# Performance work log

Measured on AMD Instinct MI355X. Metric: run time of the kernel, lower is better.

Reference implementation:

```python
import jax, jax.numpy as jnp
import numpy as np

N_E = 8192
E_DIM = 512
BETA = 0.25


def setup_inputs() -> dict:
    key = jax.random.key(0)
    k1, k2, k3, k4 = jax.random.split(key, 4)
    x = jax.random.normal(k1, (32, 512, E_DIM), dtype=jnp.float32)
    label = jax.random.randint(k2, (32, 512), 0, 100, dtype=jnp.int64)
    idx = jax.random.randint(k3, (32, 512), 0, 512, dtype=jnp.int64)
    # codebook initialized uniform(-1/n_e, 1/n_e) as in the torch module
    W = jax.random.uniform(k4, (N_E, E_DIM), dtype=jnp.float32,
                           minval=-1.0 / N_E, maxval=1.0 / N_E)
    return {"x": x, "label": label, "idx": idx, "W": W}


def reference(x, label, idx, W):
    # label/idx are unused in the forward math (mirrors the torch module)
    latent = x.reshape(-1, E_DIM)                        # [N, e_dim]
    # squared euclidean distances: ||z||^2 + ||c||^2 - 2 z c^T
    d = (jnp.sum(latent ** 2, axis=1, keepdims=True)
         + jnp.sum(W ** 2, axis=1)[None, :]
         - 2.0 * jnp.matmul(latent, W.T))                # [N, n_e]
    indices = jnp.argmin(d, axis=-1)                     # [N]
    x_q = W[indices].reshape(x.shape)                    # gather + reshape
    commitment_loss = jnp.mean((jax.lax.stop_gradient(x_q) - x) ** 2)
    loss = BETA * commitment_loss
    # straight-through estimator
    x_q = x + jax.lax.stop_gradient(x_q - x)
    indices = indices.reshape(x.shape[:-1])
    return x_q, loss, indices
```

## Files before the change

kernel.cpp:

```cpp
#include <hip/hip_runtime.h>
#include <cstdint>
#include <cstddef>

#define EDIM  512
#define NROWS 16384
#define NE    8192
#define XQSZ  (NROWS * EDIM)
#define NTILE 64
#define K3    1536

#define OFF_PART  0
#define OFF_Z     16384
#define OFF_C2    81920
#define OFF_KEYS  114688
#define OFF_TMIN  245760
#define OFF_CNT   4440064
#define OFF_LIST  4441088
#define OFF_XE    8635392
#define OFF_WE    58967040

typedef __attribute__((ext_vector_type(8)))  short          short8;
typedef __attribute__((ext_vector_type(16))) float          f32x16;
typedef __attribute__((ext_vector_type(4)))  unsigned short u16x4;

__global__ void k_rownorm(const float* __restrict__ in, float* __restrict__ out, int nrows) {
#pragma clang fp contract(off)
    int row = blockIdx.x * blockDim.x + threadIdx.x;
    if (row >= nrows) return;
    const float* p = in + (size_t)row * EDIM;
    float S[4];
#pragma unroll
    for (int b = 0; b < 4; ++b) {
        const float* q = p + b * 128;
        float r[8];
#pragma unroll
        for (int j = 0; j < 8; ++j) { float v = q[j]; r[j] = v * v; }
        for (int i = 8; i < 128; i += 8) {
#pragma unroll
            for (int j = 0; j < 8; ++j) { float v = q[i + j]; r[j] = r[j] + v * v; }
        }
        S[b] = ((r[0] + r[1]) + (r[2] + r[3])) + ((r[4] + r[5]) + (r[6] + r[7]));
    }
    out[row] = (S[0] + S[1]) + (S[2] + S[3]);
}

__device__ __forceinline__ unsigned short f2bf(float f) {
    unsigned u = __float_as_uint(f);
    return (unsigned short)((u + 0x7FFFu + ((u >> 16) & 1u)) >> 16);
}
__device__ __forceinline__ float bf2f(unsigned short h) {
    return __uint_as_float(((unsigned)h) << 16);
}

__global__ __launch_bounds__(256) void k_split3(const float* __restrict__ in,
        unsigned short* __restrict__ outp, int nrows) {
    int e = blockIdx.x * 256 + threadIdx.x;
    int row = e >> 7;
    int d0  = (e & 127) << 2;
    if (row >= nrows) return;
    float4 v = *(const float4*)(in + (size_t)row * EDIM + d0);
    float vv[4] = {v.x, v.y, v.z, v.w};
    u16x4 H, M, L;
#pragma unroll
    for (int i = 0; i < 4; ++i) {
        float f = vv[i];
        unsigned short h = f2bf(f);
        float r1 = f - bf2f(h);
        unsigned short m = f2bf(r1);
        float r2 = r1 - bf2f(m);
        L[i] = f2bf(r2); H[i] = h; M[i] = m;
    }
    unsigned short* o = outp + (size_t)row * K3 + d0;
    *(u16x4*)(o) = H; *(u16x4*)(o + EDIM) = M; *(u16x4*)(o + 2 * EDIM) = L;
}

__device__ __forceinline__ void gld16(const void* g, void* l) {
    __builtin_amdgcn_global_load_lds((const __attribute__((address_space(1))) void*)g,
                                     (__attribute__((address_space(3))) void*)l, 16, 0, 0);
}

#define GBM 128
#define GBN 128
#define GBK 64

__global__ __launch_bounds__(256) void k_argmin_hi(
        const unsigned short* __restrict__ Xe, const unsigned short* __restrict__ We,
        const float* __restrict__ c2, unsigned* __restrict__ tmin) {
    __shared__ __align__(16) unsigned short At[GBM * GBK];
    __shared__ __align__(16) unsigned short Bt[GBN * GBK];
    __shared__ unsigned smin[GBM];
    __shared__ float cs[GBN];

    const int tid = threadIdx.x;
    const int lane = tid & 63, wid = tid >> 6;
    const int wr = wid >> 1, wc = wid & 1;

    const int bid = blockIdx.x;
    const int swz = (bid & 7) * 1024 + (bid >> 3);
    const int rowtile = swz & 127, codetile = swz >> 7;
    const int row0 = rowtile * GBM, code0 = codetile * GBN;

    if (tid < GBM) smin[tid] = 0xFFFFFFFFu;
    if (tid < GBN) cs[tid] = 4.0f + c2[code0 + tid];

    f32x16 acc[2][2];
#pragma unroll
    for (int i = 0; i < 2; ++i)
#pragma unroll
        for (int j = 0; j < 2; ++j)
#pragma unroll
            for (int r = 0; r < 16; ++r) acc[i][j][r] = 0.0f;

    size_t ga[4], gb[4];
#pragma unroll
    for (int i = 0; i < 4; ++i) {
        int chunk = i * 256 + tid;
        int row   = chunk >> 3;
        int kcs   = (chunk & 7) ^ (row & 7);
        ga[i] = (size_t)(row0 + row) * K3 + kcs * 8;
        gb[i] = (size_t)(code0 + row) * K3 + kcs * 8;
    }

    const int cb0 = wr * 64 + (lane & 31);
    const int xa0 = wc * 64 + (lane & 31);
    const int kh  = lane >> 5;
    const int sb  = cb0 & 7, sa = xa0 & 7;

    for (int kt = 0; kt < EDIM / GBK; ++kt) {
        const size_t ko = (size_t)kt * GBK;
#pragma unroll
        for (int i = 0; i < 4; ++i) {
            gld16(Xe + ga[i] + ko, (char*)At + i * 4096 + wid * 1024);
            gld16(We + gb[i] + ko, (char*)Bt + i * 4096 + wid * 1024);
        }
        __syncthreads();
#pragma unroll
        for (int ks = 0; ks < 4; ++ks) {
            const int ch = ks * 2 + kh;
            short8 c0 = *(const short8*)((const char*)Bt + cb0 * 128        + ((ch ^ sb) * 16));
            short8 c1 = *(const short8*)((const char*)Bt + (cb0 + 32) * 128 + ((ch ^ sb) * 16));
            short8 x0 = *(const short8*)((const char*)At + xa0 * 128        + ((ch ^ sa) * 16));
            short8 x1 = *(const short8*)((const char*)At + (xa0 + 32) * 128 + ((ch ^ sa) * 16));
            acc[0][0] = __builtin_amdgcn_mfma_f32_32x32x16_bf16(c0, x0, acc[0][0], 0, 0, 0);
            acc[0][1] = __builtin_amdgcn_mfma_f32_32x32x16_bf16(c0, x1, acc[0][1], 0, 0, 0);
            acc[1][0] = __builtin_amdgcn_mfma_f32_32x32x16_bf16(c1, x0, acc[1][0], 0, 0, 0);
            acc[1][1] = __builtin_amdgcn_mfma_f32_32x32x16_bf16(c1, x1, acc[1][1], 0, 0, 0);
        }
        __syncthreads();
    }

    const int kh4 = kh * 4;
#pragma unroll
    for (int nj = 0; nj < 2; ++nj) {
        float dmin = 3.4e38f;
#pragma unroll
        for (int mi = 0; mi < 2; ++mi) {
#pragma unroll
            for (int q = 0; q < 4; ++q) {
                const float4 cq = *(const float4*)&cs[wr * 64 + mi * 32 + q * 8 + kh4];
                dmin = fminf(dmin, fmaf(-2.0f, acc[mi][nj][q * 4 + 0], cq.x));
                dmin = fminf(dmin, fmaf(-2.0f, acc[mi][nj][q * 4 + 1], cq.y));
                dmin = fminf(dmin, fmaf(-2.0f, acc[mi][nj][q * 4 + 2], cq.z));
                dmin = fminf(dmin, fmaf(-2.0f, acc[mi][nj][q * 4 + 3], cq.w));
            }
        }
        const int xr = wc * 64 + nj * 32 + (lane & 31);
        atomicMin(&smin[xr], __float_as_uint(dmin));
    }
    __syncthreads();
    if (tid < GBM) tmin[codetile * NROWS + row0 + tid] = smin[tid];
}

__global__ __launch_bounds__(256) void k_select(
        const unsigned* __restrict__ tmin, const float* __restrict__ Z,
        int* __restrict__ cnt, int* __restrict__ list) {
    const int row = blockIdx.x * 256 + threadIdx.x;
    unsigned mn = 0xFFFFFFFFu;
    for (int t = 0; t < NTILE; ++t) {
        unsigned v = tmin[t * NROWS + row];
        if (v < mn) mn = v;
    }
    const float margin = 4.35e-5f * sqrtf(Z[row]) + 1.7e-4f;
    const float thr = __uint_as_float(mn) + margin;
    for (int t = 0; t < NTILE; ++t) {
        if (__uint_as_float(tmin[t * NROWS + row]) <= thr) {
            int p = atomicAdd(&cnt[t], 1);
            list[t * NROWS + p] = row;
        }
    }
}

__global__ __launch_bounds__(256) void k_rescore_mfma(
        const unsigned short* __restrict__ Xe, const unsigned short* __restrict__ We,
        const float* __restrict__ Z, const float* __restrict__ c2,
        const int* __restrict__ cnt, const int* __restrict__ list,
        unsigned long long* __restrict__ keys) {
    __shared__ __align__(16) unsigned short At[GBM * GBK];
    __shared__ __align__(16) unsigned short Bt[GBN * GBK];
    __shared__ int rl_s[GBM];
    __shared__ float Zs[GBM];
    __shared__ float cs2[GBN];

    const int tile = blockIdx.x;
    const int n = cnt[tile];
    if (n == 0) return;
    const int* rows = list + tile * NROWS;
    const int tid = threadIdx.x;
    const int lane = tid & 63, wid = tid >> 6;
    const int wr = wid >> 1, wc = wid & 1;
    const int code0 = tile * 128;

    if (tid < GBN) cs2[tid] = c2[code0 + tid];

    const int cb0 = wr * 64 + (lane & 31);
    const int xa0 = wc * 64 + (lane & 31);
    const int kh  = lane >> 5;
    const int kh4 = kh * 4;
    const int sb  = cb0 & 7, sa = xa0 & 7;

    for (int chk = (int)blockIdx.y; chk * GBM < n; chk += 16) {
        __syncthreads();
        if (tid < GBM) {
            int ri = chk * GBM + tid;
            int r = rows[ri < n ? ri : 0];
            rl_s[tid] = r;
            Zs[tid] = Z[r];
        }
        __syncthreads();

        size_t aoff[4], boff[4];
#pragma unroll
        for (int i = 0; i < 4; ++i) {
            int chunk = i * 256 + tid;
            int row   = chunk >> 3;
            int kcs   = (chunk & 7) ^ (row & 7);
            aoff[i] = (size_t)rl_s[row] * K3 + kcs * 8;
            boff[i] = (size_t)(code0 + row) * K3 + kcs * 8;
        }

        f32x16 acc[2][2];
#pragma unroll
        for (int i = 0; i < 2; ++i)
#pragma unroll
            for (int j = 0; j < 2; ++j)
#pragma unroll
                for (int r = 0; r < 16; ++r) acc[i][j][r] = 0.0f;

#pragma unroll
        for (int bt = 0; bt < 6; ++bt) {
            const int ao = (bt == 1 || bt == 2) ? EDIM : (bt == 4 ? 2 * EDIM : 0);
            const int bo = (bt == 0 || bt == 2) ? EDIM : (bt == 3 ? 2 * EDIM : 0);
            for (int kc = 0; kc < 8; ++kc) {
                const int ko = ao + kc * GBK;
                const int kob = bo + kc * GBK;
#pragma unroll
                for (int i = 0; i < 4; ++i) {
                    gld16(Xe + aoff[i] + ko,  (char*)At + i * 4096 + wid * 1024);
                    gld16(We + boff[i] + kob, (char*)Bt + i * 4096 + wid * 1024);
                }
                __syncthreads();
#pragma unroll
                for (int ks = 0; ks < 4; ++ks) {
                    const int ch = ks * 2 + kh;
                    short8 c0 = *(const short8*)((const char*)Bt + cb0 * 128        + ((ch ^ sb) * 16));
                    short8 c1 = *(const short8*)((const char*)Bt + (cb0 + 32) * 128 + ((ch ^ sb) * 16));
                    short8 x0 = *(const short8*)((const char*)At + xa0 * 128        + ((ch ^ sa) * 16));
                    short8 x1 = *(const short8*)((const char*)At + (xa0 + 32) * 128 + ((ch ^ sa) * 16));
                    acc[0][0] = __builtin_amdgcn_mfma_f32_32x32x16_bf16(c0, x0, acc[0][0], 0, 0, 0);
                    acc[0][1] = __builtin_amdgcn_mfma_f32_32x32x16_bf16(c0, x1, acc[0][1], 0, 0, 0);
                    acc[1][0] = __builtin_amdgcn_mfma_f32_32x32x16_bf16(c1, x0, acc[1][0], 0, 0, 0);
                    acc[1][1] = __builtin_amdgcn_mfma_f32_32x32x16_bf16(c1, x1, acc[1][1], 0, 0, 0);
                }
                __syncthreads();
            }
        }

#pragma unroll
        for (int nj = 0; nj < 2; ++nj) {
            const int xr = wc * 64 + nj * 32 + (lane & 31);
            const float Zr = Zs[xr];
            float dm = 3.4e38f; int jm = 0;
#pragma unroll
            for (int mi = 0; mi < 2; ++mi) {
#pragma unroll
                for (int q = 0; q < 4; ++q) {
                    const float4 cq = *(const float4*)&cs2[wr * 64 + mi * 32 + q * 8 + kh4];
                    const int jb = code0 + wr * 64 + mi * 32 + q * 8 + kh4;
                    { const float d = (Zr + cq.x) - 2.0f * acc[mi][nj][q * 4 + 0];
                      if (d < dm) { dm = d; jm = jb + 0; } }
                    { const float d = (Zr + cq.y) - 2.0f * acc[mi][nj][q * 4 + 1];
                      if (d < dm) { dm = d; jm = jb + 1; } }
                    { const float d = (Zr + cq.z) - 2.0f * acc[mi][nj][q * 4 + 2];
                      if (d < dm) { dm = d; jm = jb + 2; } }
                    { const float d = (Zr + cq.w) - 2.0f * acc[mi][nj][q * 4 + 3];
                      if (d < dm) { dm = d; jm = jb + 3; } }
                }
            }
            const unsigned long long k =
                (((unsigned long long)__float_as_uint(dm)) << 13) | (unsigned)jm;
            atomicMin(&keys[rl_s[xr]], k);
        }
    }
}

__global__ __launch_bounds__(256) void k_gather(
        const float* __restrict__ x, const float* __restrict__ W,
        const unsigned long long* __restrict__ keys,
        float* __restrict__ out, double* __restrict__ part) {
    const int tid = threadIdx.x;
    const int row = blockIdx.x * 8 + (tid >> 5);
    const int c = tid & 31;
    const int idx = (int)(keys[row] & 0x1FFFull);

    const float* wrow = W + (size_t)idx * EDIM;
    const float* xrow = x + (size_t)row * EDIM;
    float* orow = out + (size_t)row * EDIM;

    double lsum = 0.0;
#pragma unroll
    for (int v = 0; v < 4; ++v) {
        const int d = c * 4 + v * 128;
        float4 xv = *(const float4*)(xrow + d);
        float4 wv = *(const float4*)(wrow + d);
        float t0 = wv.x - xv.x, t1 = wv.y - xv.y, t2 = wv.z - xv.z, t3 = wv.w - xv.w;
        float4 ov = { xv.x + t0, xv.y + t1, xv.z + t2, xv.w + t3 };
        *(float4*)(orow + d) = ov;
        lsum += (double)t0 * t0 + (double)t1 * t1 + (double)t2 * t2 + (double)t3 * t3;
    }
    if (c == 0) out[XQSZ + 1 + row] = (float)idx;

#pragma unroll
    for (int off = 32; off > 0; off >>= 1) lsum += __shfl_down(lsum, off, 64);
    __shared__ double pb[4];
    if ((tid & 63) == 0) pb[tid >> 6] = lsum;
    __syncthreads();
    if (tid == 0) part[blockIdx.x] = pb[0] + pb[1] + pb[2] + pb[3];
}

__global__ __launch_bounds__(256) void k_finalize(float* __restrict__ out,
        const double* __restrict__ part) {
    const int tid = threadIdx.x;
    double s = 0.0;
    for (int i = tid; i < 2048; i += 256) s += part[i];
#pragma unroll
    for (int off = 32; off > 0; off >>= 1) s += __shfl_down(s, off, 64);
    __shared__ double pb[4];
    if ((tid & 63) == 0) pb[tid >> 6] = s;
    __syncthreads();
    if (tid == 0) out[XQSZ] = (float)(0.25 * (pb[0] + pb[1] + pb[2] + pb[3]) / (double)XQSZ);
}

extern "C" void kernel_launch(void* const* d_in, const int* in_sizes, int n_in,
                              void* d_out, int out_size, void* d_ws, size_t ws_size,
                              hipStream_t stream) {
    const float* x = (const float*)d_in[0];
    const float* W = (const float*)d_in[3];
    float* out = (float*)d_out;
    char* ws = (char*)d_ws;

    double* part = (double*)(ws + OFF_PART);
    float* Z    = (float*)(ws + OFF_Z);
    float* c2   = (float*)(ws + OFF_C2);
    unsigned long long* keys = (unsigned long long*)(ws + OFF_KEYS);
    unsigned* tmin = (unsigned*)(ws + OFF_TMIN);
    int* cnt  = (int*)(ws + OFF_CNT);
    int* list = (int*)(ws + OFF_LIST);
    unsigned short* Xe = (unsigned short*)(ws + OFF_XE);
    unsigned short* We = (unsigned short*)(ws + OFF_WE);

    hipMemsetAsync(keys, 0xFF, NROWS * sizeof(unsigned long long), stream);
    hipMemsetAsync(cnt, 0, NTILE * sizeof(int), stream);
    k_rownorm<<<NROWS / 256, 256, 0, stream>>>(x, Z, NROWS);
    k_rownorm<<<NE / 256, 256, 0, stream>>>(W, c2, NE);
    k_split3<<<(NROWS * 128) / 256, 256, 0, stream>>>(x, Xe, NROWS);
    k_split3<<<(NE * 128) / 256, 256, 0, stream>>>(W, We, NE);
    k_argmin_hi<<<(NROWS / GBM) * (NE / GBN), 256, 0, stream>>>(Xe, We, c2, tmin);
    k_select<<<NROWS / 256, 256, 0, stream>>>(tmin, Z, cnt, list);
    k_rescore_mfma<<<dim3(NTILE, 16), 256, 0, stream>>>(Xe, We, Z, c2, cnt, list, keys);
    k_gather<<<NROWS / 8, 256, 0, stream>>>(x, W, keys, out, part);
    k_finalize<<<1, 256, 0, stream>>>(out, part);
}
```

Baseline: 535.6 us.

## Fuse prep kernels into one launch and shrink rescore row tile to 32

Merges the two row-norm and two bf16x3 split kernels into a single k_prep launch that dispatches on block index, removing three kernel launches. The rescore kernel now processes candidate rows in chunks of 32 instead of 128, with each wave owning 32 codes and a single MFMA accumulator. Its epilogue reduces packed distance/index keys with a cross-half shuffle before the atomicMin. Smaller chunks cut wasted padded work when per-tile candidate counts are small. The cost is that the codebook tile is reloaded more often per candidate row, and each MFMA has less operand reuse.

```diff
diff --git a/kernel.cpp b/kernel.cpp
--- a/kernel.cpp
+++ b/kernel.cpp
@@ -23,11 +23,8 @@
 typedef __attribute__((ext_vector_type(16))) float          f32x16;
 typedef __attribute__((ext_vector_type(4)))  unsigned short u16x4;
 
-__global__ void k_rownorm(const float* __restrict__ in, float* __restrict__ out, int nrows) {
+__device__ __forceinline__ float rownorm512(const float* __restrict__ p) {
 #pragma clang fp contract(off)
-    int row = blockIdx.x * blockDim.x + threadIdx.x;
-    if (row >= nrows) return;
-    const float* p = in + (size_t)row * EDIM;
     float S[4];
 #pragma unroll
     for (int b = 0; b < 4; ++b) {
@@ -41,7 +38,7 @@
         }
         S[b] = ((r[0] + r[1]) + (r[2] + r[3])) + ((r[4] + r[5]) + (r[6] + r[7]));
     }
-    out[row] = (S[0] + S[1]) + (S[2] + S[3]);
+    return (S[0] + S[1]) + (S[2] + S[3]);
 }
 
 __device__ __forceinline__ unsigned short f2bf(float f) {
@@ -52,12 +49,10 @@
     return __uint_as_float(((unsigned)h) << 16);
 }
 
-__global__ __launch_bounds__(256) void k_split3(const float* __restrict__ in,
-        unsigned short* __restrict__ outp, int nrows) {
-    int e = blockIdx.x * 256 + threadIdx.x;
+__device__ __forceinline__ void split_group(const float* __restrict__ in,
+        unsigned short* __restrict__ outp, int e) {
     int row = e >> 7;
     int d0  = (e & 127) << 2;
-    if (row >= nrows) return;
     float4 v = *(const float4*)(in + (size_t)row * EDIM + d0);
     float vv[4] = {v.x, v.y, v.z, v.w};
     u16x4 H, M, L;
@@ -72,6 +67,24 @@
     }
     unsigned short* o = outp + (size_t)row * K3 + d0;
     *(u16x4*)(o) = H; *(u16x4*)(o + EDIM) = M; *(u16x4*)(o + 2 * EDIM) = L;
+}
+
+__global__ __launch_bounds__(256) void k_prep(
+        const float* __restrict__ x, const float* __restrict__ W,
+        unsigned short* __restrict__ Xe, unsigned short* __restrict__ We,
+        float* __restrict__ Z, float* __restrict__ c2) {
+    const int bid = blockIdx.x, tid = threadIdx.x;
+    if (bid < 8192) {
+        split_group(x, Xe, bid * 256 + tid);
+    } else if (bid < 12288) {
+        split_group(W, We, (bid - 8192) * 256 + tid);
+    } else if (bid < 12352) {
+        const int row = (bid - 12288) * 256 + tid;
+        Z[row] = rownorm512(x + (size_t)row * EDIM);
+    } else {
+        const int row = (bid - 12352) * 256 + tid;
+        c2[row] = rownorm512(W + (size_t)row * EDIM);
+    }
 }
 
 __device__ __forceinline__ void gld16(const void* g, void* l) {
@@ -195,10 +208,11 @@
         const float* __restrict__ Z, const float* __restrict__ c2,
         const int* __restrict__ cnt, const int* __restrict__ list,
         unsigned long long* __restrict__ keys) {
-    __shared__ __align__(16) unsigned short At[GBM * GBK];
+#define RBM 32
+    __shared__ __align__(16) unsigned short At[RBM * GBK];
     __shared__ __align__(16) unsigned short Bt[GBN * GBK];
-    __shared__ int rl_s[GBM];
-    __shared__ float Zs[GBM];
+    __shared__ int rl_s[RBM];
+    __shared__ float Zs[RBM];
     __shared__ float cs2[GBN];
 
     const int tile = blockIdx.x;
@@ -207,100 +221,81 @@
     const int* rows = list + tile * NROWS;
     const int tid = threadIdx.x;
     const int lane = tid & 63, wid = tid >> 6;
-    const int wr = wid >> 1, wc = wid & 1;
     const int code0 = tile * 128;
 
     if (tid < GBN) cs2[tid] = c2[code0 + tid];
 
-    const int cb0 = wr * 64 + (lane & 31);
-    const int xa0 = wc * 64 + (lane & 31);
-    const int kh  = lane >> 5;
-    const int kh4 = kh * 4;
-    const int sb  = cb0 & 7, sa = xa0 & 7;
-
-    for (int chk = (int)blockIdx.y; chk * GBM < n; chk += 16) {
+    const int cb = wid * 32 + (lane & 31);
+    const int xa = lane & 31;
+    const int kh = lane >> 5;
+    const int sb = cb & 7, sa = xa & 7;
+
+    size_t boff[4];
+#pragma unroll
+    for (int i = 0; i < 4; ++i) {
+        int chunk = i * 256 + tid;
+        int brow  = chunk >> 3;
+        int bkcs  = (chunk & 7) ^ (brow & 7);
+        boff[i] = (size_t)(code0 + brow) * K3 + bkcs * 8;
+    }
+    const int arow = tid >> 3;
+    const int akcs = (tid & 7) ^ (arow & 7);
+
+    for (int chk = (int)blockIdx.y; chk * RBM < n; chk += 16) {
         __syncthreads();
-        if (tid < GBM) {
-            int ri = chk * GBM + tid;
+        if (tid < RBM) {
+            int ri = chk * RBM + tid;
             int r = rows[ri < n ? ri : 0];
             rl_s[tid] = r;
             Zs[tid] = Z[r];
         }
         __syncthreads();
 
-        size_t aoff[4], boff[4];
-#pragma unroll
-        for (int i = 0; i < 4; ++i) {
-            int chunk = i * 256 + tid;
-            int row   = chunk >> 3;
-            int kcs   = (chunk & 7) ^ (row & 7);
-            aoff[i] = (size_t)rl_s[row] * K3 + kcs * 8;
-            boff[i] = (size_t)(code0 + row) * K3 + kcs * 8;
-        }
-
-        f32x16 acc[2][2];
-#pragma unroll
-        for (int i = 0; i < 2; ++i)
-#pragma unroll
-            for (int j = 0; j < 2; ++j)
-#pragma unroll
-                for (int r = 0; r < 16; ++r) acc[i][j][r] = 0.0f;
+        const size_t aoff = (size_t)rl_s[arow] * K3 + akcs * 8;
+
+        f32x16 acc;
+#pragma unroll
+        for (int r = 0; r < 16; ++r) acc[r] = 0.0f;
 
 #pragma unroll
         for (int bt = 0; bt < 6; ++bt) {
             const int ao = (bt == 1 || bt == 2) ? EDIM : (bt == 4 ? 2 * EDIM : 0);
             const int bo = (bt == 0 || bt == 2) ? EDIM : (bt == 3 ? 2 * EDIM : 0);
             for (int kc = 0; kc < 8; ++kc) {
-                const int ko = ao + kc * GBK;
-                const int kob = bo + kc * GBK;
-#pragma unroll
-                for (int i = 0; i < 4; ++i) {
-                    gld16(Xe + aoff[i] + ko,  (char*)At + i * 4096 + wid * 1024);
-                    gld16(We + boff[i] + kob, (char*)Bt + i * 4096 + wid * 1024);
-                }
+                gld16(Xe + aoff + ao + kc * GBK, (char*)At + wid * 1024);
+#pragma unroll
+                for (int i = 0; i < 4; ++i)
+                    gld16(We + boff[i] + bo + kc * GBK, (char*)Bt + i * 4096 + wid * 1024);
                 __syncthreads();
 #pragma unroll
                 for (int ks = 0; ks < 4; ++ks) {
                     const int ch = ks * 2 + kh;
-                    short8 c0 = *(const short8*)((const char*)Bt + cb0 * 128        + ((ch ^ sb) * 16));
-                    short8 c1 = *(const short8*)((const char*)Bt + (cb0 + 32) * 128 + ((ch ^ sb) * 16));
-                    short8 x0 = *(const short8*)((const char*)At + xa0 * 128        + ((ch ^ sa) * 16));
-                    short8 x1 = *(const short8*)((const char*)At + (xa0 + 32) * 128 + ((ch ^ sa) * 16));
-                    acc[0][0] = __builtin_amdgcn_mfma_f32_32x32x16_bf16(c0, x0, acc[0][0], 0, 0, 0);
-                    acc[0][1] = __builtin_amdgcn_mfma_f32_32x32x16_bf16(c0, x1, acc[0][1], 0, 0, 0);
-                    acc[1][0] = __builtin_amdgcn_mfma_f32_32x32x16_bf16(c1, x0, acc[1][0], 0, 0, 0);
-                    acc[1][1] = __builtin_amdgcn_mfma_f32_32x32x16_bf16(c1, x1, acc[1][1], 0, 0, 0);
+                    short8 cf = *(const short8*)((const char*)Bt + cb * 128 + ((ch ^ sb) * 16));
+                    short8 xf = *(const short8*)((const char*)At + xa * 128 + ((ch ^ sa) * 16));
+                    acc = __builtin_amdgcn_mfma_f32_32x32x16_bf16(cf, xf, acc, 0, 0, 0);
                 }
                 __syncthreads();
             }
         }
 
-#pragma unroll
-        for (int nj = 0; nj < 2; ++nj) {
-            const int xr = wc * 64 + nj * 32 + (lane & 31);
-            const float Zr = Zs[xr];
-            float dm = 3.4e38f; int jm = 0;
-#pragma unroll
-            for (int mi = 0; mi < 2; ++mi) {
-#pragma unroll
-                for (int q = 0; q < 4; ++q) {
-                    const float4 cq = *(const float4*)&cs2[wr * 64 + mi * 32 + q * 8 + kh4];
-                    const int jb = code0 + wr * 64 + mi * 32 + q * 8 + kh4;
-                    { const float d = (Zr + cq.x) - 2.0f * acc[mi][nj][q * 4 + 0];
-                      if (d < dm) { dm = d; jm = jb + 0; } }
-                    { const float d = (Zr + cq.y) - 2.0f * acc[mi][nj][q * 4 + 1];
-                      if (d < dm) { dm = d; jm = jb + 1; } }
-                    { const float d = (Zr + cq.z) - 2.0f * acc[mi][nj][q * 4 + 2];
-                      if (d < dm) { dm = d; jm = jb + 2; } }
-                    { const float d = (Zr + cq.w) - 2.0f * acc[mi][nj][q * 4 + 3];
-                      if (d < dm) { dm = d; jm = jb + 3; } }
-                }
-            }
-            const unsigned long long k =
-                (((unsigned long long)__float_as_uint(dm)) << 13) | (unsigned)jm;
-            atomicMin(&keys[rl_s[xr]], k);
-        }
-    }
+        const float Zr = Zs[xa];
+        unsigned long long k = ~0ull;
+#pragma unroll
+        for (int reg = 0; reg < 16; ++reg) {
+            const int crow = (reg & 3) + 8 * (reg >> 2) + 4 * kh;
+            const float d = (Zr + cs2[wid * 32 + crow]) - 2.0f * acc[reg];
+            const unsigned long long kk =
+                (((unsigned long long)__float_as_uint(d)) << 13)
+                | (unsigned)(code0 + wid * 32 + crow);
+            if (kk < k) k = kk;
+        }
+        {
+            unsigned long long o = __shfl_xor(k, 32, 64);
+            if (o < k) k = o;
+        }
+        if (lane < 32) atomicMin(&keys[rl_s[xa]], k);
+    }
+#undef RBM
 }
 
 __global__ __launch_bounds__(256) void k_gather(
@@ -370,10 +365,7 @@
 
     hipMemsetAsync(keys, 0xFF, NROWS * sizeof(unsigned long long), stream);
     hipMemsetAsync(cnt, 0, NTILE * sizeof(int), stream);
-    k_rownorm<<<NROWS / 256, 256, 0, stream>>>(x, Z, NROWS);
-    k_rownorm<<<NE / 256, 256, 0, stream>>>(W, c2, NE);
-    k_split3<<<(NROWS * 128) / 256, 256, 0, stream>>>(x, Xe, NROWS);
-    k_split3<<<(NE * 128) / 256, 256, 0, stream>>>(W, We, NE);
+    k_prep<<<12384, 256, 0, stream>>>(x, W, Xe, We, Z, c2);
     k_argmin_hi<<<(NROWS / GBM) * (NE / GBN), 256, 0, stream>>>(Xe, We, c2, tmin);
     k_select<<<NROWS / 256, 256, 0, stream>>>(tmin, Z, cnt, list);
     k_rescore_mfma<<<dim3(NTILE, 16), 256, 0, stream>>>(Xe, We, Z, c2, cnt, list, keys);
```

Result: slower. 634.9 us (+18.5%).

## Fuse prep kernels into one launch and double-buffer rescore MFMA loads

Applied to the files above, without the earlier changes.

Merges the two rownorm and two split3 launches into a single k_prep kernel that dispatches on block index. In the rescore kernel, the LDS tiles are double-buffered, with explicit vmcnt waits and barriers, so the global-to-LDS loads for the next stage overlap the MFMAs of the current one. B offsets are hoisted out of the chunk loop. This cuts launch overhead and load latency stalls, at the cost of doubled shared memory in rescore and hand-written waitcnt sequencing that must match the number of loads in flight.

```diff
diff --git a/kernel.cpp b/kernel.cpp
--- a/kernel.cpp
+++ b/kernel.cpp
@@ -23,11 +23,8 @@
 typedef __attribute__((ext_vector_type(16))) float          f32x16;
 typedef __attribute__((ext_vector_type(4)))  unsigned short u16x4;
 
-__global__ void k_rownorm(const float* __restrict__ in, float* __restrict__ out, int nrows) {
+__device__ __forceinline__ float rownorm512(const float* __restrict__ p) {
 #pragma clang fp contract(off)
-    int row = blockIdx.x * blockDim.x + threadIdx.x;
-    if (row >= nrows) return;
-    const float* p = in + (size_t)row * EDIM;
     float S[4];
 #pragma unroll
     for (int b = 0; b < 4; ++b) {
@@ -41,7 +38,7 @@
         }
         S[b] = ((r[0] + r[1]) + (r[2] + r[3])) + ((r[4] + r[5]) + (r[6] + r[7]));
     }
-    out[row] = (S[0] + S[1]) + (S[2] + S[3]);
+    return (S[0] + S[1]) + (S[2] + S[3]);
 }
 
 __device__ __forceinline__ unsigned short f2bf(float f) {
@@ -52,12 +49,10 @@
     return __uint_as_float(((unsigned)h) << 16);
 }
 
-__global__ __launch_bounds__(256) void k_split3(const float* __restrict__ in,
-        unsigned short* __restrict__ outp, int nrows) {
-    int e = blockIdx.x * 256 + threadIdx.x;
+__device__ __forceinline__ void split_group(const float* __restrict__ in,
+        unsigned short* __restrict__ outp, int e) {
     int row = e >> 7;
     int d0  = (e & 127) << 2;
-    if (row >= nrows) return;
     float4 v = *(const float4*)(in + (size_t)row * EDIM + d0);
     float vv[4] = {v.x, v.y, v.z, v.w};
     u16x4 H, M, L;
@@ -72,6 +67,24 @@
     }
     unsigned short* o = outp + (size_t)row * K3 + d0;
     *(u16x4*)(o) = H; *(u16x4*)(o + EDIM) = M; *(u16x4*)(o + 2 * EDIM) = L;
+}
+
+__global__ __launch_bounds__(256) void k_prep(
+        const float* __restrict__ x, const float* __restrict__ W,
+        unsigned short* __restrict__ Xe, unsigned short* __restrict__ We,
+        float* __restrict__ Z, float* __restrict__ c2) {
+    const int bid = blockIdx.x, tid = threadIdx.x;
+    if (bid < 8192) {
+        split_group(x, Xe, bid * 256 + tid);
+    } else if (bid < 12288) {
+        split_group(W, We, (bid - 8192) * 256 + tid);
+    } else if (bid < 12352) {
+        const int row = (bid - 12288) * 256 + tid;
+        Z[row] = rownorm512(x + (size_t)row * EDIM);
+    } else {
+        const int row = (bid - 12352) * 256 + tid;
+        c2[row] = rownorm512(W + (size_t)row * EDIM);
+    }
 }
 
 __device__ __forceinline__ void gld16(const void* g, void* l) {
@@ -195,8 +208,8 @@
         const float* __restrict__ Z, const float* __restrict__ c2,
         const int* __restrict__ cnt, const int* __restrict__ list,
         unsigned long long* __restrict__ keys) {
-    __shared__ __align__(16) unsigned short At[GBM * GBK];
-    __shared__ __align__(16) unsigned short Bt[GBN * GBK];
+    __shared__ __align__(16) unsigned short At[2][GBM * GBK];
+    __shared__ __align__(16) unsigned short Bt[2][GBN * GBK];
     __shared__ int rl_s[GBM];
     __shared__ float Zs[GBM];
     __shared__ float cs2[GBN];
@@ -218,6 +231,41 @@
     const int kh4 = kh * 4;
     const int sb  = cb0 & 7, sa = xa0 & 7;
 
+    size_t boff[4];
+    int arow4[4], akcs4[4];
+#pragma unroll
+    for (int i = 0; i < 4; ++i) {
+        int chunk = i * 256 + tid;
+        int row   = chunk >> 3;
+        int kcs   = (chunk & 7) ^ (row & 7);
+        arow4[i] = row; akcs4[i] = kcs;
+        boff[i] = (size_t)(code0 + row) * K3 + kcs * 8;
+    }
+
+#define RSTAGE(ss, bb) { \
+        const int bt_ = (ss) >> 3, kc_ = (ss) & 7; \
+        const int ao_ = (bt_ == 1 || bt_ == 2) ? EDIM : (bt_ == 4 ? 2 * EDIM : 0); \
+        const int bo_ = (bt_ == 0 || bt_ == 2) ? EDIM : (bt_ == 3 ? 2 * EDIM : 0); \
+        _Pragma("unroll") \
+        for (int i_ = 0; i_ < 4; ++i_) { \
+            gld16(Xe + aoff[i_] + ao_ + kc_ * GBK, (char*)At[bb] + i_ * 4096 + wid * 1024); \
+            gld16(We + boff[i_] + bo_ + kc_ * GBK, (char*)Bt[bb] + i_ * 4096 + wid * 1024); \
+        } }
+
+#define RCOMP(bb) { \
+        _Pragma("unroll") \
+        for (int ks_ = 0; ks_ < 4; ++ks_) { \
+            const int ch_ = ks_ * 2 + kh; \
+            short8 cf0 = *(const short8*)((const char*)Bt[bb] + cb0 * 128        + ((ch_ ^ sb) * 16)); \
+            short8 cf1 = *(const short8*)((const char*)Bt[bb] + (cb0 + 32) * 128 + ((ch_ ^ sb) * 16)); \
+            short8 xf0 = *(const short8*)((const char*)At[bb] + xa0 * 128        + ((ch_ ^ sa) * 16)); \
+            short8 xf1 = *(const short8*)((const char*)At[bb] + (xa0 + 32) * 128 + ((ch_ ^ sa) * 16)); \
+            acc[0][0] = __builtin_amdgcn_mfma_f32_32x32x16_bf16(cf0, xf0, acc[0][0], 0, 0, 0); \
+            acc[0][1] = __builtin_amdgcn_mfma_f32_32x32x16_bf16(cf0, xf1, acc[0][1], 0, 0, 0); \
+            acc[1][0] = __builtin_amdgcn_mfma_f32_32x32x16_bf16(cf1, xf0, acc[1][0], 0, 0, 0); \
+            acc[1][1] = __builtin_amdgcn_mfma_f32_32x32x16_bf16(cf1, xf1, acc[1][1], 0, 0, 0); \
+        } }
+
     for (int chk = (int)blockIdx.y; chk * GBM < n; chk += 16) {
         __syncthreads();
         if (tid < GBM) {
@@ -228,15 +276,10 @@
         }
         __syncthreads();
 
-        size_t aoff[4], boff[4];
-#pragma unroll
-        for (int i = 0; i < 4; ++i) {
-            int chunk = i * 256 + tid;
-            int row   = chunk >> 3;
-            int kcs   = (chunk & 7) ^ (row & 7);
-            aoff[i] = (size_t)rl_s[row] * K3 + kcs * 8;
-            boff[i] = (size_t)(code0 + row) * K3 + kcs * 8;
-        }
+        size_t aoff[4];
+#pragma unroll
+        for (int i = 0; i < 4; ++i)
+            aoff[i] = (size_t)rl_s[arow4[i]] * K3 + akcs4[i] * 8;
 
         f32x16 acc[2][2];
 #pragma unroll
@@ -246,34 +289,18 @@
 #pragma unroll
                 for (int r = 0; r < 16; ++r) acc[i][j][r] = 0.0f;
 
-#pragma unroll
-        for (int bt = 0; bt < 6; ++bt) {
-            const int ao = (bt == 1 || bt == 2) ? EDIM : (bt == 4 ? 2 * EDIM : 0);
-            const int bo = (bt == 0 || bt == 2) ? EDIM : (bt == 3 ? 2 * EDIM : 0);
-            for (int kc = 0; kc < 8; ++kc) {
-                const int ko = ao + kc * GBK;
-                const int kob = bo + kc * GBK;
-#pragma unroll
-                for (int i = 0; i < 4; ++i) {
-                    gld16(Xe + aoff[i] + ko,  (char*)At + i * 4096 + wid * 1024);
-                    gld16(We + boff[i] + kob, (char*)Bt + i * 4096 + wid * 1024);
-                }
-                __syncthreads();
-#pragma unroll
-                for (int ks = 0; ks < 4; ++ks) {
-                    const int ch = ks * 2 + kh;
-                    short8 c0 = *(const short8*)((const char*)Bt + cb0 * 128        + ((ch ^ sb) * 16));
-                    short8 c1 = *(const short8*)((const char*)Bt + (cb0 + 32) * 128 + ((ch ^ sb) * 16));
-                    short8 x0 = *(const short8*)((const char*)At + xa0 * 128        + ((ch ^ sa) * 16));
-                    short8 x1 = *(const short8*)((const char*)At + (xa0 + 32) * 128 + ((ch ^ sa) * 16));
-                    acc[0][0] = __builtin_amdgcn_mfma_f32_32x32x16_bf16(c0, x0, acc[0][0], 0, 0, 0);
-                    acc[0][1] = __builtin_amdgcn_mfma_f32_32x32x16_bf16(c0, x1, acc[0][1], 0, 0, 0);
-                    acc[1][0] = __builtin_amdgcn_mfma_f32_32x32x16_bf16(c1, x0, acc[1][0], 0, 0, 0);
-                    acc[1][1] = __builtin_amdgcn_mfma_f32_32x32x16_bf16(c1, x1, acc[1][1], 0, 0, 0);
-                }
-                __syncthreads();
-            }
-        }
+        RSTAGE(0, 0);
+#pragma unroll 1
+        for (int s = 0; s < 47; ++s) {
+            RSTAGE(s + 1, (s + 1) & 1);
+            asm volatile("s_waitcnt vmcnt(8)" ::: "memory");
+            asm volatile("s_barrier" ::: "memory");
+            RCOMP(s & 1);
+            asm volatile("s_barrier" ::: "memory");
+        }
+        asm volatile("s_waitcnt vmcnt(0)" ::: "memory");
+        asm volatile("s_barrier" ::: "memory");
+        RCOMP(1);
 
 #pragma unroll
         for (int nj = 0; nj < 2; ++nj) {
@@ -301,6 +328,8 @@
             atomicMin(&keys[rl_s[xr]], k);
         }
     }
+#undef RSTAGE
+#undef RCOMP
 }
 
 __global__ __launch_bounds__(256) void k_gather(
@@ -370,10 +399,7 @@
 
     hipMemsetAsync(keys, 0xFF, NROWS * sizeof(unsigned long long), stream);
     hipMemsetAsync(cnt, 0, NTILE * sizeof(int), stream);
-    k_rownorm<<<NROWS / 256, 256, 0, stream>>>(x, Z, NROWS);
-    k_rownorm<<<NE / 256, 256, 0, stream>>>(W, c2, NE);
-    k_split3<<<(NROWS * 128) / 256, 256, 0, stream>>>(x, Xe, NROWS);
-    k_split3<<<(NE * 128) / 256, 256, 0, stream>>>(W, We, NE);
+    k_prep<<<12384, 256, 0, stream>>>(x, W, Xe, We, Z, c2);
     k_argmin_hi<<<(NROWS / GBM) * (NE / GBN), 256, 0, stream>>>(Xe, We, c2, tmin);
     k_select<<<NROWS / 256, 256, 0, stream>>>(tmin, Z, cnt, list);
     k_rescore_mfma<<<dim3(NTILE, 16), 256, 0, stream>>>(Xe, We, Z, c2, cnt, list, keys);
```

Result: slower. 567.3 us (+5.9%).
